# Optimization experiments

Measured on AMD Instinct MI355X. Metric: run time of the kernel, lower is better.

The kernel has to match this reference:

```python
import jax, jax.numpy as jnp
import numpy as np

D_MODEL, D_K, D_V = 512, 64, 64
LN_EPS = 1e-6


def setup_inputs() -> dict:
    key = jax.random.key(0)
    ks = jax.random.split(key, 8)
    B, Lq, Lk = 2, 1024, 1024
    q = jax.random.normal(ks[0], (B, Lq, D_MODEL), dtype=jnp.float32)
    k = jax.random.normal(ks[1], (B, Lk, D_MODEL), dtype=jnp.float32)
    v = jax.random.normal(ks[2], (B, Lk, D_MODEL), dtype=jnp.float32)
    s = 1.0 / np.sqrt(D_MODEL)
    Wq = jax.random.normal(ks[3], (D_MODEL, D_K), dtype=jnp.float32) * s
    Wk = jax.random.normal(ks[4], (D_MODEL, D_K), dtype=jnp.float32) * s
    Wv = jax.random.normal(ks[5], (D_MODEL, D_V), dtype=jnp.float32) * s
    v_param = jax.random.normal(ks[6], (D_K,), dtype=jnp.float32)
    Wfc = jax.random.normal(ks[7], (D_V, D_MODEL), dtype=jnp.float32) / np.sqrt(D_V)
    ln_gamma = jnp.ones((D_MODEL,), dtype=jnp.float32)
    ln_beta = jnp.zeros((D_MODEL,), dtype=jnp.float32)
    return {"q": q, "k": k, "v": v, "Wq": Wq, "Wk": Wk, "Wv": Wv,
            "v_param": v_param, "Wfc": Wfc, "ln_gamma": ln_gamma, "ln_beta": ln_beta}


def reference(q, k, v, Wq, Wk, Wv, v_param, Wfc, ln_gamma, ln_beta):
    residual = q
    qp = q @ Wq                      # [B, Lq, d_k]
    kp = k @ Wk                      # [B, Lk, d_k]
    vp = v @ Wv                      # [B, Lk, d_v]
    # additive (Bahdanau) scores: tanh(q_i + k_j) . v_param  -> [B, Lq, Lk]
    scores = jnp.einsum("bqkd,d->bqk", jnp.tanh(qp[:, :, None, :] + kp[:, None, :, :]), v_param)
    attn = jax.nn.softmax(scores, axis=-1)   # dropout is identity in eval mode
    out = jnp.einsum("bqk,bkv->bqv", attn, vp)
    out = out @ Wfc + residual               # [B, Lq, d_model]
    mu = jnp.mean(out, axis=-1, keepdims=True)
    var = jnp.var(out, axis=-1, keepdims=True)
    out = (out - mu) * jax.lax.rsqrt(var + LN_EPS) * ln_gamma + ln_beta
    return out, attn
```

## Files before the change

kernel.cpp:

```cpp
#include <hip/hip_runtime.h>
#include <cstddef>
#include <cstdint>

#define D_MODEL 512
#define DK 64
#define LQ 1024
#define LK 1024
#define NB 2
#define LN_EPS 1e-6f
#define L2E2 2.8853900817779268f

#define PR_ROWS 16
__global__ __launch_bounds__(256, 4) void proj_kernel(
    const float* __restrict__ q, const float* __restrict__ k,
    const float* __restrict__ v, const float* __restrict__ Wq,
    const float* __restrict__ Wk, const float* __restrict__ Wv,
    const float* __restrict__ v_param, float4* __restrict__ ab4,
    float2* __restrict__ ekT2, float* __restrict__ vp) {
  __shared__ float rows[PR_ROWS][D_MODEL];
  const int tid = threadIdx.x;
  const int type = blockIdx.x >> 7;
  const int r0 = (blockIdx.x & 127) * PR_ROWS;
  const float* __restrict__ in = (type == 0) ? q : (type == 1) ? k : v;
  const float* __restrict__ W = (type == 0) ? Wq : (type == 1) ? Wk : Wv;
  {
    const float4* __restrict__ in4 = (const float4*)(in + (size_t)r0 * D_MODEL);
    float4* r4 = (float4*)&rows[0][0];
#pragma unroll
    for (int t = 0; t < 8; ++t) r4[tid + 256 * t] = in4[tid + 256 * t];
  }
  __syncthreads();
  const int lane = tid & 63;
  const int wv = tid >> 6;
  const int rglob = r0 + wv * 4;
  const float* __restrict__ Wl = W + lane;
  float c0[4] = {0.f, 0.f, 0.f, 0.f}, c1[4] = {0.f, 0.f, 0.f, 0.f};
#pragma unroll 4
  for (int e = 0; e < D_MODEL; e += 4) {
    float w0 = Wl[(size_t)(e + 0) * DK];
    float w1 = Wl[(size_t)(e + 1) * DK];
    float w2 = Wl[(size_t)(e + 2) * DK];
    float w3 = Wl[(size_t)(e + 3) * DK];
#pragma unroll
    for (int r = 0; r < 4; ++r) {
      float4 x = *(const float4*)&rows[wv * 4 + r][e];
      c0[r] = fmaf(x.x, w0, c0[r]);
      c1[r] = fmaf(x.y, w1, c1[r]);
      c0[r] = fmaf(x.z, w2, c0[r]);
      c1[r] = fmaf(x.w, w3, c1[r]);
    }
  }
  float acc[4];
#pragma unroll
  for (int r = 0; r < 4; ++r) acc[r] = c0[r] + c1[r];
  if (type == 0) {
    float vpar = v_param[lane];
#pragma unroll
    for (int r = 0; r < 4; ++r) {
      float iv = __builtin_amdgcn_exp2f(-L2E2 * acc[r]);
      float A = vpar * iv, B = iv;
      float Ah = __shfl_down(A, 32);
      float Bh = __shfl_down(B, 32);
      if (lane < 32)
        ab4[(size_t)(rglob + r) * 32 + lane] = make_float4(A, B, Ah, Bh);
    }
  } else if (type == 1) {
    float e4[4], h4[4];
#pragma unroll
    for (int r = 0; r < 4; ++r) {
      e4[r] = __builtin_amdgcn_exp2f(L2E2 * acc[r]);
      h4[r] = __shfl_down(e4[r], 32);
    }
    if (lane < 32) {
      int b = rglob >> 10, j0 = rglob & 1023;
      float2* bp = ekT2 + (size_t)b * 32 * LK + (size_t)lane * LK + j0;
      *(float4*)bp = make_float4(e4[0], h4[0], e4[1], h4[1]);
      *(float4*)(bp + 2) = make_float4(e4[2], h4[2], e4[3], h4[3]);
    }
  } else {
#pragma unroll
    for (int r = 0; r < 4; ++r) vp[(size_t)(rglob + r) * DK + lane] = acc[r];
  }
}

#define RB 4
__global__ __launch_bounds__(256, 4) void attn_kernel(
    const float4* __restrict__ ab4, const float2* __restrict__ ekT2,
    const float* __restrict__ vp, const float* __restrict__ resid,
    const float* __restrict__ Wfc, const float* __restrict__ gamma,
    const float* __restrict__ beta, float* __restrict__ out,
    float* __restrict__ attn_out) {
  __shared__ float sc[RB][LK];
  __shared__ float4 pvred[4][RB][16];
  __shared__ __align__(16) float ovlT[DK][RB];
  __shared__ float red[2][RB][4];
  __shared__ float mred[RB][4], sred[RB][4];
  const int tid = threadIdx.x;
  const int row0 = blockIdx.x * RB;
  const int batch = row0 >> 10;
  const float2* __restrict__ ekT_b = ekT2 + (size_t)batch * 32 * LK + tid;
  const float* __restrict__ vp_b = vp + (size_t)batch * LK * DK;
  const float4* __restrict__ abr0 = ab4 + (size_t)(row0 + 0) * 32;
  const float4* __restrict__ abr1 = ab4 + (size_t)(row0 + 1) * 32;
  const float4* __restrict__ abr2 = ab4 + (size_t)(row0 + 2) * 32;
  const float4* __restrict__ abr3 = ab4 + (size_t)(row0 + 3) * 32;

  float a0[4] = {0.f, 0.f, 0.f, 0.f};
  float a1[4] = {0.f, 0.f, 0.f, 0.f};
  float a2[4] = {0.f, 0.f, 0.f, 0.f};
  float a3[4] = {0.f, 0.f, 0.f, 0.f};

#pragma unroll
  for (int qd = 0; qd < 16; ++qd) {
    float2 k0[4], k1[4];
#pragma unroll
    for (int jj = 0; jj < 4; ++jj) {
      k0[jj] = ekT_b[(size_t)(2 * qd + 0) * LK + jj * 256];
      k1[jj] = ekT_b[(size_t)(2 * qd + 1) * LK + jj * 256];
    }
    float4 P0 = abr0[2 * qd], Q0 = abr0[2 * qd + 1];
    float4 P1 = abr1[2 * qd], Q1 = abr1[2 * qd + 1];
    float4 P2 = abr2[2 * qd], Q2 = abr2[2 * qd + 1];
    float4 P3 = abr3[2 * qd], Q3 = abr3[2 * qd + 1];
#pragma unroll
    for (int jj = 0; jj < 4; ++jj) {
#define QUAD(PP, QQ, ACC)                                                  \
  {                                                                        \
    float x1 = k0[jj].x + PP.y, x2 = k0[jj].y + PP.w;                      \
    float x3 = k1[jj].x + QQ.y, x4 = k1[jj].y + QQ.w;                      \
    float p12 = x1 * x2, p34 = x3 * x4;                                    \
    float n12 = fmaf(PP.z, x1, PP.x * x2);                                 \
    float n34 = fmaf(QQ.z, x3, QQ.x * x4);                                 \
    float num = fmaf(n34, p12, n12 * p34);                                 \
    ACC[jj] = fmaf(num, __builtin_amdgcn_rcpf(p12 * p34), ACC[jj]);        \
  }
      QUAD(P0, Q0, a0)
      QUAD(P1, Q1, a1)
      QUAD(P2, Q2, a2)
      QUAD(P3, Q3, a3)
#undef QUAD
    }
  }

  const int wave = __builtin_amdgcn_readfirstlane(tid >> 6);
  const int lane = tid & 63;

  {
    float pm0 = fminf(fminf(a0[0], a0[1]), fminf(a0[2], a0[3]));
    float pm1 = fminf(fminf(a1[0], a1[1]), fminf(a1[2], a1[3]));
    float pm2 = fminf(fminf(a2[0], a2[1]), fminf(a2[2], a2[3]));
    float pm3 = fminf(fminf(a3[0], a3[1]), fminf(a3[2], a3[3]));
#pragma unroll
    for (int off = 32; off > 0; off >>= 1) {
      pm0 = fminf(pm0, __shfl_xor(pm0, off));
      pm1 = fminf(pm1, __shfl_xor(pm1, off));
      pm2 = fminf(pm2, __shfl_xor(pm2, off));
      pm3 = fminf(pm3, __shfl_xor(pm3, off));
    }
    if (lane == 0) {
      mred[0][wave] = pm0; mred[1][wave] = pm1;
      mred[2][wave] = pm2; mred[3][wave] = pm3;
    }
    __syncthreads();
    float m0 = fminf(fminf(mred[0][0], mred[0][1]), fminf(mred[0][2], mred[0][3]));
    float m1 = fminf(fminf(mred[1][0], mred[1][1]), fminf(mred[1][2], mred[1][3]));
    float m2 = fminf(fminf(mred[2][0], mred[2][1]), fminf(mred[2][2], mred[2][3]));
    float m3 = fminf(fminf(mred[3][0], mred[3][1]), fminf(mred[3][2], mred[3][3]));
    float s0 = 0.f, s1 = 0.f, s2 = 0.f, s3 = 0.f;
#pragma unroll
    for (int jj = 0; jj < 4; ++jj) {
      a0[jj] = __builtin_amdgcn_exp2f((m0 - a0[jj]) * L2E2); s0 += a0[jj];
      a1[jj] = __builtin_amdgcn_exp2f((m1 - a1[jj]) * L2E2); s1 += a1[jj];
      a2[jj] = __builtin_amdgcn_exp2f((m2 - a2[jj]) * L2E2); s2 += a2[jj];
      a3[jj] = __builtin_amdgcn_exp2f((m3 - a3[jj]) * L2E2); s3 += a3[jj];
    }
#pragma unroll
    for (int off = 32; off > 0; off >>= 1) {
      s0 += __shfl_xor(s0, off); s1 += __shfl_xor(s1, off);
      s2 += __shfl_xor(s2, off); s3 += __shfl_xor(s3, off);
    }
    if (lane == 0) {
      sred[0][wave] = s0; sred[1][wave] = s1;
      sred[2][wave] = s2; sred[3][wave] = s3;
    }
    __syncthreads();
    float i0 = __builtin_amdgcn_rcpf(sred[0][0] + sred[0][1] + sred[0][2] + sred[0][3]);
    float i1 = __builtin_amdgcn_rcpf(sred[1][0] + sred[1][1] + sred[1][2] + sred[1][3]);
    float i2 = __builtin_amdgcn_rcpf(sred[2][0] + sred[2][1] + sred[2][2] + sred[2][3]);
    float i3 = __builtin_amdgcn_rcpf(sred[3][0] + sred[3][1] + sred[3][2] + sred[3][3]);
    float* __restrict__ ar0 = attn_out + (size_t)(row0 + 0) * LK;
    float* __restrict__ ar1 = attn_out + (size_t)(row0 + 1) * LK;
    float* __restrict__ ar2 = attn_out + (size_t)(row0 + 2) * LK;
    float* __restrict__ ar3 = attn_out + (size_t)(row0 + 3) * LK;
#pragma unroll
    for (int jj = 0; jj < 4; ++jj) {
      float p0 = a0[jj] * i0, p1 = a1[jj] * i1;
      float p2 = a2[jj] * i2, p3 = a3[jj] * i3;
      sc[0][tid + jj * 256] = p0; ar0[tid + jj * 256] = p0;
      sc[1][tid + jj * 256] = p1; ar1[tid + jj * 256] = p1;
      sc[2][tid + jj * 256] = p2; ar2[tid + jj * 256] = p2;
      sc[3][tid + jj * 256] = p3; ar3[tid + jj * 256] = p3;
    }
  }
  __syncthreads();

  {
    const int jj = lane >> 4, l16 = lane & 15;
    const float4* __restrict__ vp4 = (const float4*)vp_b;
    float4 a[RB];
#pragma unroll
    for (int r = 0; r < RB; ++r) a[r] = make_float4(0.f, 0.f, 0.f, 0.f);
#pragma unroll 4
    for (int it = 0; it < 64; ++it) {
      int j = (wave << 8) + (it << 2) + jj;
      float4 vv = vp4[(size_t)j * (DK / 4) + l16];
#pragma unroll
      for (int r = 0; r < RB; ++r) {
        float pw = sc[r][j];
        a[r].x = fmaf(pw, vv.x, a[r].x);
        a[r].y = fmaf(pw, vv.y, a[r].y);
        a[r].z = fmaf(pw, vv.z, a[r].z);
        a[r].w = fmaf(pw, vv.w, a[r].w);
      }
    }
#pragma unroll
    for (int r = 0; r < RB; ++r) {
      a[r].x += __shfl_xor(a[r].x, 16); a[r].y += __shfl_xor(a[r].y, 16);
      a[r].z += __shfl_xor(a[r].z, 16); a[r].w += __shfl_xor(a[r].w, 16);
      a[r].x += __shfl_xor(a[r].x, 32); a[r].y += __shfl_xor(a[r].y, 32);
      a[r].z += __shfl_xor(a[r].z, 32); a[r].w += __shfl_xor(a[r].w, 32);
    }
    if (jj == 0) {
#pragma unroll
      for (int r = 0; r < RB; ++r) pvred[wave][r][l16] = a[r];
    }
  }
  __syncthreads();
  if (tid < 64) {
    int r = tid >> 4, l16 = tid & 15;
    float4 s = make_float4(0.f, 0.f, 0.f, 0.f);
#pragma unroll
    for (int w = 0; w < 4; ++w) {
      float4 t = pvred[w][r][l16];
      s.x += t.x; s.y += t.y; s.z += t.z; s.w += t.w;
    }
    ovlT[l16 * 4 + 0][r] = s.x;
    ovlT[l16 * 4 + 1][r] = s.y;
    ovlT[l16 * 4 + 2][r] = s.z;
    ovlT[l16 * 4 + 3][r] = s.w;
  }
  __syncthreads();

  {
    const int c0 = tid, c1 = tid + 256;
    float y[RB][2];
#pragma unroll
    for (int r = 0; r < RB; ++r) {
      y[r][0] = resid[(size_t)(row0 + r) * D_MODEL + c0];
      y[r][1] = resid[(size_t)(row0 + r) * D_MODEL + c1];
    }
#pragma unroll 4
    for (int e = 0; e < DK; ++e) {
      float w0 = Wfc[(size_t)e * D_MODEL + c0];
      float w1 = Wfc[(size_t)e * D_MODEL + c1];
      float4 ov = *(const float4*)&ovlT[e][0];
      y[0][0] = fmaf(ov.x, w0, y[0][0]); y[0][1] = fmaf(ov.x, w1, y[0][1]);
      y[1][0] = fmaf(ov.y, w0, y[1][0]); y[1][1] = fmaf(ov.y, w1, y[1][1]);
      y[2][0] = fmaf(ov.z, w0, y[2][0]); y[2][1] = fmaf(ov.z, w1, y[2][1]);
      y[3][0] = fmaf(ov.w, w0, y[3][0]); y[3][1] = fmaf(ov.w, w1, y[3][1]);
    }
#pragma unroll
    for (int r = 0; r < RB; ++r) {
      float s = y[r][0] + y[r][1];
#pragma unroll
      for (int off = 32; off > 0; off >>= 1) s += __shfl_xor(s, off);
      if (lane == 0) red[0][r][wave] = s;
    }
    __syncthreads();
    float mu[RB];
#pragma unroll
    for (int r = 0; r < RB; ++r)
      mu[r] = (red[0][r][0] + red[0][r][1] + red[0][r][2] + red[0][r][3]) *
              (1.0f / D_MODEL);
#pragma unroll
    for (int r = 0; r < RB; ++r) {
      float d0 = y[r][0] - mu[r], d1 = y[r][1] - mu[r];
      float s = d0 * d0 + d1 * d1;
#pragma unroll
      for (int off = 32; off > 0; off >>= 1) s += __shfl_xor(s, off);
      if (lane == 0) red[1][r][wave] = s;
    }
    __syncthreads();
    float g0 = gamma[c0], g1 = gamma[c1], b0 = beta[c0], b1 = beta[c1];
#pragma unroll
    for (int r = 0; r < RB; ++r) {
      float var = (red[1][r][0] + red[1][r][1] + red[1][r][2] + red[1][r][3]) *
                  (1.0f / D_MODEL);
      float rstd = rsqrtf(var + LN_EPS);
      out[(size_t)(row0 + r) * D_MODEL + c0] = (y[r][0] - mu[r]) * rstd * g0 + b0;
      out[(size_t)(row0 + r) * D_MODEL + c1] = (y[r][1] - mu[r]) * rstd * g1 + b1;
    }
  }
}

extern "C" void kernel_launch(void* const* d_in, const int* in_sizes, int n_in,
                              void* d_out, int out_size, void* d_ws,
                              size_t ws_size, hipStream_t stream) {
  const float* q = (const float*)d_in[0];
  const float* k = (const float*)d_in[1];
  const float* v = (const float*)d_in[2];
  const float* Wq = (const float*)d_in[3];
  const float* Wk = (const float*)d_in[4];
  const float* Wv = (const float*)d_in[5];
  const float* v_param = (const float*)d_in[6];
  const float* Wfc = (const float*)d_in[7];
  const float* gamma = (const float*)d_in[8];
  const float* beta = (const float*)d_in[9];

  float* out = (float*)d_out;
  float* attn = out + (size_t)NB * LQ * D_MODEL;

  float* base = (float*)d_ws;
  float4* ab4 = (float4*)base;
  float* p1 = base + (size_t)NB * LQ * 32 * 4;
  float2* ekT2 = (float2*)p1;
  float* vp = p1 + (size_t)NB * 32 * LK * 2;

  hipLaunchKernelGGL(proj_kernel, dim3(3 * 128), dim3(256), 0, stream, q, k, v,
                     Wq, Wk, Wv, v_param, ab4, ekT2, vp);
  hipLaunchKernelGGL(attn_kernel, dim3(NB * LQ / RB), dim3(256), 0, stream,
                     ab4, ekT2, vp, q, Wfc, gamma, beta, out, attn);
}
```

Baseline: 54.46 us.

## Double attn block to 512 threads and read projection inputs directly from global

The attention kernel now uses 512 threads per block, so each thread handles 2 key columns instead of 4. The P·V reduction spans 8 waves and each thread produces one LayerNorm column instead of two. The aim is more parallelism and fewer serial score computations per thread, at the cost of larger cross-wave reductions and more redundant per-row loads. Separately, the projection kernel drops its shared-memory staging and barrier, reading each wave's four input rows straight from global memory with wave-uniform addresses. This relies on cache broadcast instead of LDS reuse.

```diff
diff --git a/kernel.cpp b/kernel.cpp
--- a/kernel.cpp
+++ b/kernel.cpp
@@ -17,23 +17,19 @@
     const float* __restrict__ Wk, const float* __restrict__ Wv,
     const float* __restrict__ v_param, float4* __restrict__ ab4,
     float2* __restrict__ ekT2, float* __restrict__ vp) {
-  __shared__ float rows[PR_ROWS][D_MODEL];
   const int tid = threadIdx.x;
   const int type = blockIdx.x >> 7;
   const int r0 = (blockIdx.x & 127) * PR_ROWS;
   const float* __restrict__ in = (type == 0) ? q : (type == 1) ? k : v;
   const float* __restrict__ W = (type == 0) ? Wq : (type == 1) ? Wk : Wv;
-  {
-    const float4* __restrict__ in4 = (const float4*)(in + (size_t)r0 * D_MODEL);
-    float4* r4 = (float4*)&rows[0][0];
-#pragma unroll
-    for (int t = 0; t < 8; ++t) r4[tid + 256 * t] = in4[tid + 256 * t];
-  }
-  __syncthreads();
   const int lane = tid & 63;
-  const int wv = tid >> 6;
+  const int wv = __builtin_amdgcn_readfirstlane(tid >> 6);
   const int rglob = r0 + wv * 4;
   const float* __restrict__ Wl = W + lane;
+  const float* __restrict__ rp0 = in + (size_t)(rglob + 0) * D_MODEL;
+  const float* __restrict__ rp1 = in + (size_t)(rglob + 1) * D_MODEL;
+  const float* __restrict__ rp2 = in + (size_t)(rglob + 2) * D_MODEL;
+  const float* __restrict__ rp3 = in + (size_t)(rglob + 3) * D_MODEL;
   float c0[4] = {0.f, 0.f, 0.f, 0.f}, c1[4] = {0.f, 0.f, 0.f, 0.f};
 #pragma unroll 4
   for (int e = 0; e < D_MODEL; e += 4) {
@@ -41,14 +37,18 @@
     float w1 = Wl[(size_t)(e + 1) * DK];
     float w2 = Wl[(size_t)(e + 2) * DK];
     float w3 = Wl[(size_t)(e + 3) * DK];
-#pragma unroll
-    for (int r = 0; r < 4; ++r) {
-      float4 x = *(const float4*)&rows[wv * 4 + r][e];
-      c0[r] = fmaf(x.x, w0, c0[r]);
-      c1[r] = fmaf(x.y, w1, c1[r]);
-      c0[r] = fmaf(x.z, w2, c0[r]);
-      c1[r] = fmaf(x.w, w3, c1[r]);
-    }
+    float4 x0 = *(const float4*)&rp0[e];
+    float4 x1 = *(const float4*)&rp1[e];
+    float4 x2 = *(const float4*)&rp2[e];
+    float4 x3 = *(const float4*)&rp3[e];
+    c0[0] = fmaf(x0.x, w0, c0[0]); c1[0] = fmaf(x0.y, w1, c1[0]);
+    c0[0] = fmaf(x0.z, w2, c0[0]); c1[0] = fmaf(x0.w, w3, c1[0]);
+    c0[1] = fmaf(x1.x, w0, c0[1]); c1[1] = fmaf(x1.y, w1, c1[1]);
+    c0[1] = fmaf(x1.z, w2, c0[1]); c1[1] = fmaf(x1.w, w3, c1[1]);
+    c0[2] = fmaf(x2.x, w0, c0[2]); c1[2] = fmaf(x2.y, w1, c1[2]);
+    c0[2] = fmaf(x2.z, w2, c0[2]); c1[2] = fmaf(x2.w, w3, c1[2]);
+    c0[3] = fmaf(x3.x, w0, c0[3]); c1[3] = fmaf(x3.y, w1, c1[3]);
+    c0[3] = fmaf(x3.z, w2, c0[3]); c1[3] = fmaf(x3.w, w3, c1[3]);
   }
   float acc[4];
 #pragma unroll
@@ -84,17 +84,17 @@
 }
 
 #define RB 4
-__global__ __launch_bounds__(256, 4) void attn_kernel(
+__global__ __launch_bounds__(512, 4) void attn_kernel(
     const float4* __restrict__ ab4, const float2* __restrict__ ekT2,
     const float* __restrict__ vp, const float* __restrict__ resid,
     const float* __restrict__ Wfc, const float* __restrict__ gamma,
     const float* __restrict__ beta, float* __restrict__ out,
     float* __restrict__ attn_out) {
   __shared__ float sc[RB][LK];
-  __shared__ float4 pvred[4][RB][16];
+  __shared__ float4 pvred[8][RB][16];
   __shared__ __align__(16) float ovlT[DK][RB];
-  __shared__ float red[2][RB][4];
-  __shared__ float mred[RB][4], sred[RB][4];
+  __shared__ float red[2][RB][8];
+  __shared__ float mred[RB][8], sred[RB][8];
   const int tid = threadIdx.x;
   const int row0 = blockIdx.x * RB;
   const int batch = row0 >> 10;
@@ -105,25 +105,24 @@
   const float4* __restrict__ abr2 = ab4 + (size_t)(row0 + 2) * 32;
   const float4* __restrict__ abr3 = ab4 + (size_t)(row0 + 3) * 32;
 
-  float a0[4] = {0.f, 0.f, 0.f, 0.f};
-  float a1[4] = {0.f, 0.f, 0.f, 0.f};
-  float a2[4] = {0.f, 0.f, 0.f, 0.f};
-  float a3[4] = {0.f, 0.f, 0.f, 0.f};
+  float a0[2] = {0.f, 0.f};
+  float a1[2] = {0.f, 0.f};
+  float a2[2] = {0.f, 0.f};
+  float a3[2] = {0.f, 0.f};
 
 #pragma unroll
   for (int qd = 0; qd < 16; ++qd) {
-    float2 k0[4], k1[4];
-#pragma unroll
-    for (int jj = 0; jj < 4; ++jj) {
-      k0[jj] = ekT_b[(size_t)(2 * qd + 0) * LK + jj * 256];
-      k1[jj] = ekT_b[(size_t)(2 * qd + 1) * LK + jj * 256];
-    }
+    float2 k0[2], k1[2];
+    k0[0] = ekT_b[(size_t)(2 * qd + 0) * LK];
+    k1[0] = ekT_b[(size_t)(2 * qd + 1) * LK];
+    k0[1] = ekT_b[(size_t)(2 * qd + 0) * LK + 512];
+    k1[1] = ekT_b[(size_t)(2 * qd + 1) * LK + 512];
     float4 P0 = abr0[2 * qd], Q0 = abr0[2 * qd + 1];
     float4 P1 = abr1[2 * qd], Q1 = abr1[2 * qd + 1];
     float4 P2 = abr2[2 * qd], Q2 = abr2[2 * qd + 1];
     float4 P3 = abr3[2 * qd], Q3 = abr3[2 * qd + 1];
 #pragma unroll
-    for (int jj = 0; jj < 4; ++jj) {
+    for (int jj = 0; jj < 2; ++jj) {
 #define QUAD(PP, QQ, ACC)                                                  \
   {                                                                        \
     float x1 = k0[jj].x + PP.y, x2 = k0[jj].y + PP.w;                      \
@@ -146,10 +145,10 @@
   const int lane = tid & 63;
 
   {
-    float pm0 = fminf(fminf(a0[0], a0[1]), fminf(a0[2], a0[3]));
-    float pm1 = fminf(fminf(a1[0], a1[1]), fminf(a1[2], a1[3]));
-    float pm2 = fminf(fminf(a2[0], a2[1]), fminf(a2[2], a2[3]));
-    float pm3 = fminf(fminf(a3[0], a3[1]), fminf(a3[2], a3[3]));
+    float pm0 = fminf(a0[0], a0[1]);
+    float pm1 = fminf(a1[0], a1[1]);
+    float pm2 = fminf(a2[0], a2[1]);
+    float pm3 = fminf(a3[0], a3[1]);
 #pragma unroll
     for (int off = 32; off > 0; off >>= 1) {
       pm0 = fminf(pm0, __shfl_xor(pm0, off));
@@ -162,13 +161,15 @@
       mred[2][wave] = pm2; mred[3][wave] = pm3;
     }
     __syncthreads();
-    float m0 = fminf(fminf(mred[0][0], mred[0][1]), fminf(mred[0][2], mred[0][3]));
-    float m1 = fminf(fminf(mred[1][0], mred[1][1]), fminf(mred[1][2], mred[1][3]));
-    float m2 = fminf(fminf(mred[2][0], mred[2][1]), fminf(mred[2][2], mred[2][3]));
-    float m3 = fminf(fminf(mred[3][0], mred[3][1]), fminf(mred[3][2], mred[3][3]));
+    float m0 = 1e30f, m1 = 1e30f, m2 = 1e30f, m3 = 1e30f;
+#pragma unroll
+    for (int w = 0; w < 8; ++w) {
+      m0 = fminf(m0, mred[0][w]); m1 = fminf(m1, mred[1][w]);
+      m2 = fminf(m2, mred[2][w]); m3 = fminf(m3, mred[3][w]);
+    }
     float s0 = 0.f, s1 = 0.f, s2 = 0.f, s3 = 0.f;
 #pragma unroll
-    for (int jj = 0; jj < 4; ++jj) {
+    for (int jj = 0; jj < 2; ++jj) {
       a0[jj] = __builtin_amdgcn_exp2f((m0 - a0[jj]) * L2E2); s0 += a0[jj];
       a1[jj] = __builtin_amdgcn_exp2f((m1 - a1[jj]) * L2E2); s1 += a1[jj];
       a2[jj] = __builtin_amdgcn_exp2f((m2 - a2[jj]) * L2E2); s2 += a2[jj];
@@ -184,22 +185,28 @@
       sred[2][wave] = s2; sred[3][wave] = s3;
     }
     __syncthreads();
-    float i0 = __builtin_amdgcn_rcpf(sred[0][0] + sred[0][1] + sred[0][2] + sred[0][3]);
-    float i1 = __builtin_amdgcn_rcpf(sred[1][0] + sred[1][1] + sred[1][2] + sred[1][3]);
-    float i2 = __builtin_amdgcn_rcpf(sred[2][0] + sred[2][1] + sred[2][2] + sred[2][3]);
-    float i3 = __builtin_amdgcn_rcpf(sred[3][0] + sred[3][1] + sred[3][2] + sred[3][3]);
+    float t0 = 0.f, t1 = 0.f, t2 = 0.f, t3 = 0.f;
+#pragma unroll
+    for (int w = 0; w < 8; ++w) {
+      t0 += sred[0][w]; t1 += sred[1][w];
+      t2 += sred[2][w]; t3 += sred[3][w];
+    }
+    float i0 = __builtin_amdgcn_rcpf(t0);
+    float i1 = __builtin_amdgcn_rcpf(t1);
+    float i2 = __builtin_amdgcn_rcpf(t2);
+    float i3 = __builtin_amdgcn_rcpf(t3);
     float* __restrict__ ar0 = attn_out + (size_t)(row0 + 0) * LK;
     float* __restrict__ ar1 = attn_out + (size_t)(row0 + 1) * LK;
     float* __restrict__ ar2 = attn_out + (size_t)(row0 + 2) * LK;
     float* __restrict__ ar3 = attn_out + (size_t)(row0 + 3) * LK;
 #pragma unroll
-    for (int jj = 0; jj < 4; ++jj) {
+    for (int jj = 0; jj < 2; ++jj) {
       float p0 = a0[jj] * i0, p1 = a1[jj] * i1;
       float p2 = a2[jj] * i2, p3 = a3[jj] * i3;
-      sc[0][tid + jj * 256] = p0; ar0[tid + jj * 256] = p0;
-      sc[1][tid + jj * 256] = p1; ar1[tid + jj * 256] = p1;
-      sc[2][tid + jj * 256] = p2; ar2[tid + jj * 256] = p2;
-      sc[3][tid + jj * 256] = p3; ar3[tid + jj * 256] = p3;
+      sc[0][tid + jj * 512] = p0; ar0[tid + jj * 512] = p0;
+      sc[1][tid + jj * 512] = p1; ar1[tid + jj * 512] = p1;
+      sc[2][tid + jj * 512] = p2; ar2[tid + jj * 512] = p2;
+      sc[3][tid + jj * 512] = p3; ar3[tid + jj * 512] = p3;
     }
   }
   __syncthreads();
@@ -211,8 +218,8 @@
 #pragma unroll
     for (int r = 0; r < RB; ++r) a[r] = make_float4(0.f, 0.f, 0.f, 0.f);
 #pragma unroll 4
-    for (int it = 0; it < 64; ++it) {
-      int j = (wave << 8) + (it << 2) + jj;
+    for (int it = 0; it < 32; ++it) {
+      int j = (wave << 7) + (it << 2) + jj;
       float4 vv = vp4[(size_t)j * (DK / 4) + l16];
 #pragma unroll
       for (int r = 0; r < RB; ++r) {
@@ -240,7 +247,7 @@
     int r = tid >> 4, l16 = tid & 15;
     float4 s = make_float4(0.f, 0.f, 0.f, 0.f);
 #pragma unroll
-    for (int w = 0; w < 4; ++w) {
+    for (int w = 0; w < 8; ++w) {
       float4 t = pvred[w][r][l16];
       s.x += t.x; s.y += t.y; s.z += t.z; s.w += t.w;
     }
@@ -252,26 +259,23 @@
   __syncthreads();
 
   {
-    const int c0 = tid, c1 = tid + 256;
-    float y[RB][2];
-#pragma unroll
-    for (int r = 0; r < RB; ++r) {
-      y[r][0] = resid[(size_t)(row0 + r) * D_MODEL + c0];
-      y[r][1] = resid[(size_t)(row0 + r) * D_MODEL + c1];
-    }
+    const int c = tid;
+    float y[RB];
+#pragma unroll
+    for (int r = 0; r < RB; ++r)
+      y[r] = resid[(size_t)(row0 + r) * D_MODEL + c];
 #pragma unroll 4
     for (int e = 0; e < DK; ++e) {
-      float w0 = Wfc[(size_t)e * D_MODEL + c0];
-      float w1 = Wfc[(size_t)e * D_MODEL + c1];
+      float w = Wfc[(size_t)e * D_MODEL + c];
       float4 ov = *(const float4*)&ovlT[e][0];
-      y[0][0] = fmaf(ov.x, w0, y[0][0]); y[0][1] = fmaf(ov.x, w1, y[0][1]);
-      y[1][0] = fmaf(ov.y, w0, y[1][0]); y[1][1] = fmaf(ov.y, w1, y[1][1]);
-      y[2][0] = fmaf(ov.z, w0, y[2][0]); y[2][1] = fmaf(ov.z, w1, y[2][1]);
-      y[3][0] = fmaf(ov.w, w0, y[3][0]); y[3][1] = fmaf(ov.w, w1, y[3][1]);
-    }
-#pragma unroll
-    for (int r = 0; r < RB; ++r) {
-      float s = y[r][0] + y[r][1];
+      y[0] = fmaf(ov.x, w, y[0]);
+      y[1] = fmaf(ov.y, w, y[1]);
+      y[2] = fmaf(ov.z, w, y[2]);
+      y[3] = fmaf(ov.w, w, y[3]);
+    }
+#pragma unroll
+    for (int r = 0; r < RB; ++r) {
+      float s = y[r];
 #pragma unroll
       for (int off = 32; off > 0; off >>= 1) s += __shfl_xor(s, off);
       if (lane == 0) red[0][r][wave] = s;
@@ -279,26 +283,30 @@
     __syncthreads();
     float mu[RB];
 #pragma unroll
-    for (int r = 0; r < RB; ++r)
-      mu[r] = (red[0][r][0] + red[0][r][1] + red[0][r][2] + red[0][r][3]) *
-              (1.0f / D_MODEL);
-#pragma unroll
-    for (int r = 0; r < RB; ++r) {
-      float d0 = y[r][0] - mu[r], d1 = y[r][1] - mu[r];
-      float s = d0 * d0 + d1 * d1;
+    for (int r = 0; r < RB; ++r) {
+      float s = 0.f;
+#pragma unroll
+      for (int w = 0; w < 8; ++w) s += red[0][r][w];
+      mu[r] = s * (1.0f / D_MODEL);
+    }
+#pragma unroll
+    for (int r = 0; r < RB; ++r) {
+      float d = y[r] - mu[r];
+      float s = d * d;
 #pragma unroll
       for (int off = 32; off > 0; off >>= 1) s += __shfl_xor(s, off);
       if (lane == 0) red[1][r][wave] = s;
     }
     __syncthreads();
-    float g0 = gamma[c0], g1 = gamma[c1], b0 = beta[c0], b1 = beta[c1];
-#pragma unroll
-    for (int r = 0; r < RB; ++r) {
-      float var = (red[1][r][0] + red[1][r][1] + red[1][r][2] + red[1][r][3]) *
-                  (1.0f / D_MODEL);
+    float gg = gamma[c], bb = beta[c];
+#pragma unroll
+    for (int r = 0; r < RB; ++r) {
+      float s = 0.f;
+#pragma unroll
+      for (int w = 0; w < 8; ++w) s += red[1][r][w];
+      float var = s * (1.0f / D_MODEL);
       float rstd = rsqrtf(var + LN_EPS);
-      out[(size_t)(row0 + r) * D_MODEL + c0] = (y[r][0] - mu[r]) * rstd * g0 + b0;
-      out[(size_t)(row0 + r) * D_MODEL + c1] = (y[r][1] - mu[r]) * rstd * g1 + b1;
+      out[(size_t)(row0 + r) * D_MODEL + c] = (y[r] - mu[r]) * rstd * gg + bb;
     }
   }
 }
@@ -328,6 +336,6 @@
 
   hipLaunchKernelGGL(proj_kernel, dim3(3 * 128), dim3(256), 0, stream, q, k, v,
                      Wq, Wk, Wv, v_param, ab4, ekT2, vp);
-  hipLaunchKernelGGL(attn_kernel, dim3(NB * LQ / RB), dim3(256), 0, stream,
+  hipLaunchKernelGGL(attn_kernel, dim3(NB * LQ / RB), dim3(512), 0, stream,
                      ab4, ekT2, vp, q, Wfc, gamma, beta, out, attn);
 }
```

After: 61.12 us. 1.12x slower.
